# Kernel optimization log

Hardware: AMD Instinct MI355X
Metric: run time of the kernel (lower is better)

## Reference

```python
import jax, jax.numpy as jnp
import numpy as np

GROUP = 128  # quantization group size along the input dimension


def dequant(q, scales, zeros):
    # q: [out, in] int4 codes stored as int32 in [0,16)
    # scales, zeros: [out, in//GROUP] per-group affine params
    out_dim, in_dim = q.shape
    g = in_dim // GROUP
    w = (q.astype(jnp.float32).reshape(out_dim, g, GROUP) - zeros[:, :, None]) * scales[:, :, None]
    return w.reshape(out_dim, in_dim)


def setup_inputs() -> dict:
    key = jax.random.key(0)
    ks = jax.random.split(key, 10)
    H, I = 4096, 11008
    B, S = 64, 1
    inp = {
        "x": jax.random.normal(ks[0], (B, S, H), dtype=jnp.float32),
        "gate_qweight": jax.random.randint(ks[1], (I, H), 0, 16, dtype=jnp.int32),
        "gate_scales": jax.random.uniform(ks[2], (I, H // GROUP), dtype=jnp.float32) * 0.02,
        "gate_zeros": jax.random.uniform(ks[3], (I, H // GROUP), dtype=jnp.float32) * 16.0,
        "up_qweight": jax.random.randint(ks[4], (I, H), 0, 16, dtype=jnp.int32),
        "up_scales": jax.random.uniform(ks[5], (I, H // GROUP), dtype=jnp.float32) * 0.02,
        "up_zeros": jax.random.uniform(ks[6], (I, H // GROUP), dtype=jnp.float32) * 16.0,
        "down_qweight": jax.random.randint(ks[7], (H, I), 0, 16, dtype=jnp.int32),
        "down_scales": jax.random.uniform(ks[8], (H, I // GROUP), dtype=jnp.float32) * 0.02,
        "down_zeros": jax.random.uniform(ks[9], (H, I // GROUP), dtype=jnp.float32) * 16.0,
    }
    return inp


def reference(x, gate_qweight, gate_scales, gate_zeros,
              up_qweight, up_scales, up_zeros,
              down_qweight, down_scales, down_zeros):
    Wg = dequant(gate_qweight, gate_scales, gate_zeros)   # [I, H]
    Wu = dequant(up_qweight, up_scales, up_zeros)         # [I, H]
    Wd = dequant(down_qweight, down_scales, down_zeros)   # [H, I]
    gate = jnp.einsum('bsh,ih->bsi', x, Wg)
    up = jnp.einsum('bsh,ih->bsi', x, Wu)
    h = jax.nn.silu(gate) * up                             # SwiGLU
    return jnp.einsum('bsi,hi->bsh', h, Wd)
```

## Files before the change

kernel.cpp:

```cpp
#include <hip/hip_runtime.h>
#include <hip/hip_bf16.h>
#include <stdint.h>

#define H_DIM 4096
#define I_DIM 11008
#define NGH   32
#define NGI   86
#define KWH   512
#define KWI   1376
#define NWV   5636096

typedef __attribute__((ext_vector_type(8))) short short8;
typedef __attribute__((ext_vector_type(4))) short s16x4;
typedef __attribute__((ext_vector_type(4))) float f32x4;
typedef __attribute__((ext_vector_type(4))) int   i32x4;

static __device__ __forceinline__ short f2bf(float f) {
  union { __hip_bfloat16 b; short s; } u;
  u.b = __float2bfloat16(f);
  return u.s;
}

__global__ void xcvt_kernel(const float* __restrict__ x, short* __restrict__ xb) {
  int i = (blockIdx.x * 256 + threadIdx.x) * 4;
  f32x4 v = *(const f32x4*)(x + i);
  s16x4 o;
  o[0] = f2bf(v[0]); o[1] = f2bf(v[1]); o[2] = f2bf(v[2]); o[3] = f2bf(v[3]);
  *(s16x4*)(xb + i) = o;
}

__global__ __launch_bounds__(256) void packt_kernel(
    const int* __restrict__ gq, const int* __restrict__ uq, const int* __restrict__ dq,
    int* __restrict__ pkt) {
  __shared__ unsigned short sb[16][72];
  int bid = blockIdx.x;
  const int* src; int RL, KW; size_t obase; int rt, ct;
  if (bid < 11008) {
    src = gq; RL = H_DIM; KW = KWH; obase = 0;
    rt = bid >> 4; ct = bid & 15;
  } else if (bid < 22016) {
    src = uq; RL = H_DIM; KW = KWH; obase = (size_t)NWV;
    bid -= 11008; rt = bid >> 4; ct = bid & 15;
  } else {
    src = dq; RL = I_DIM; KW = KWI; obase = 2 * (size_t)NWV;
    bid -= 22016; rt = bid / 43; ct = bid - rt * 43;
  }
  const int t = threadIdx.x;
  const int rowl = t >> 4, j = t & 15;
  const int* rp = src + (size_t)(rt * 16 + rowl) * RL + ct * 256;
#pragma unroll
  for (int p = 0; p < 4; ++p) {
    i32x4 v = *(const i32x4*)(rp + p * 64 + j * 4);
    sb[rowl][p * 16 + j] = (unsigned short)((v[0] & 15) | ((v[1] & 15) << 4)
                        | ((v[2] & 15) << 8) | ((v[3] & 15) << 12));
  }
  __syncthreads();
  int* dst = pkt + obase + ((size_t)rt * KW + ct * 32) * 16;
#pragma unroll
  for (int p = 0; p < 2; ++p) {
    const int wi = t + p * 256;
    const int kwl = wi >> 4, ri = wi & 15;
    dst[wi] = (int)sb[ri][2 * kwl] | ((int)sb[ri][2 * kwl + 1] << 16);
  }
}

__global__ __launch_bounds__(512, 4) void phase1p_kernel(
    const short* __restrict__ xb, const int* __restrict__ pkt,
    const float* __restrict__ gsc, const float* __restrict__ gze,
    const float* __restrict__ usc, const float* __restrict__ uze,
    short* __restrict__ hb)
{
  __shared__ float red[8][4][4][64];
  const int rt   = blockIdx.x;
  const int n0   = rt * 16;
  const int w    = threadIdx.x >> 6;
  const int l    = threadIdx.x & 63;
  const int col  = l & 15;
  const int krow = l >> 4;
  const int i    = n0 + col;

  const int* gB = pkt + (size_t)rt * (KWH * 16) + col;
  const int* uB = pkt + (size_t)NWV + (size_t)rt * (KWH * 16) + col;

  float sgv[4], zgv[4], suv[4], zuv[4];
#pragma unroll
  for (int g = 0; g < 4; ++g) {
    const int gg = w * 4 + g;
    sgv[g] = gsc[(size_t)i * NGH + gg];
    zgv[g] = gze[(size_t)i * NGH + gg] * sgv[g];
    suv[g] = usc[(size_t)i * NGH + gg];
    zuv[g] = uze[(size_t)i * NGH + gg] * suv[g];
  }

  f32x4 accG[4], accU[4];
#pragma unroll
  for (int c = 0; c < 4; ++c)
#pragma unroll
    for (int r = 0; r < 4; ++r) { accG[c][r] = 0.f; accU[c][r] = 0.f; }

  const int wb  = w * 64;
  const int ks0 = w * 512 + krow * 8;

  int qgA = gB[(wb + krow) * 16], quA = uB[(wb + krow) * 16];
  int qgB_, quB_;
  short8 aA[4], aB[4];
#pragma unroll
  for (int c = 0; c < 4; ++c)
    aA[c] = *(const short8*)(xb + (size_t)(c * 16 + col) * H_DIM + ks0);

#pragma unroll
  for (int u = 0; u < 8; ++u) {
    const int t1 = 2 * u + 1;
    const int t2 = (2 * u + 2) & 15;
    const int g  = u >> 1;
    qgB_ = gB[(wb + 4 * t1 + krow) * 16];
    quB_ = uB[(wb + 4 * t1 + krow) * 16];
#pragma unroll
    for (int c = 0; c < 4; ++c)
      aB[c] = *(const short8*)(xb + (size_t)(c * 16 + col) * H_DIM + ks0 + t1 * 32);
    {
      short8 bg, bu;
#pragma unroll
      for (int j = 0; j < 8; ++j) {
        bg[j] = f2bf((float)((qgA >> (4 * j)) & 15) * sgv[g] - zgv[g]);
        bu[j] = f2bf((float)((quA >> (4 * j)) & 15) * suv[g] - zuv[g]);
      }
#pragma unroll
      for (int c = 0; c < 4; ++c) {
        accG[c] = __builtin_amdgcn_mfma_f32_16x16x32_bf16(aA[c], bg, accG[c], 0, 0, 0);
        accU[c] = __builtin_amdgcn_mfma_f32_16x16x32_bf16(aA[c], bu, accU[c], 0, 0, 0);
      }
    }
    qgA = gB[(wb + 4 * t2 + krow) * 16];
    quA = uB[(wb + 4 * t2 + krow) * 16];
#pragma unroll
    for (int c = 0; c < 4; ++c)
      aA[c] = *(const short8*)(xb + (size_t)(c * 16 + col) * H_DIM + ks0 + t2 * 32);
    {
      short8 bg, bu;
#pragma unroll
      for (int j = 0; j < 8; ++j) {
        bg[j] = f2bf((float)((qgB_ >> (4 * j)) & 15) * sgv[g] - zgv[g]);
        bu[j] = f2bf((float)((quB_ >> (4 * j)) & 15) * suv[g] - zuv[g]);
      }
#pragma unroll
      for (int c = 0; c < 4; ++c) {
        accG[c] = __builtin_amdgcn_mfma_f32_16x16x32_bf16(aB[c], bg, accG[c], 0, 0, 0);
        accU[c] = __builtin_amdgcn_mfma_f32_16x16x32_bf16(aB[c], bu, accU[c], 0, 0, 0);
      }
    }
  }

  const int c2 = threadIdx.x >> 7;
  const int rh = (threadIdx.x >> 6) & 1;
  const int ll = threadIdx.x & 63;

#pragma unroll
  for (int c = 0; c < 4; ++c)
#pragma unroll
    for (int r = 0; r < 4; ++r)
      red[w][c][r][l] = accG[c][r];
  __syncthreads();
  float gsum[2];
#pragma unroll
  for (int rr = 0; rr < 2; ++rr) {
    const int r = rh * 2 + rr;
    float s = 0.f;
#pragma unroll
    for (int ww = 0; ww < 8; ++ww) s += red[ww][c2][r][ll];
    gsum[rr] = s;
  }
  __syncthreads();

#pragma unroll
  for (int c = 0; c < 4; ++c)
#pragma unroll
    for (int r = 0; r < 4; ++r)
      red[w][c][r][l] = accU[c][r];
  __syncthreads();
#pragma unroll
  for (int rr = 0; rr < 2; ++rr) {
    const int r = rh * 2 + rr;
    float us = 0.f;
#pragma unroll
    for (int ww = 0; ww < 8; ++ww) us += red[ww][c2][r][ll];
    const float gv = gsum[rr];
    const float hv = gv / (1.f + __expf(-gv)) * us;
    const int m  = c2 * 16 + (ll >> 4) * 4 + r;
    const int ii = n0 + (ll & 15);
    hb[(size_t)m * I_DIM + ii] = f2bf(hv);
  }
}

__global__ __launch_bounds__(512, 4) void phase2p_kernel(
    const short* __restrict__ hb, const int* __restrict__ dpt,
    const float* __restrict__ dsc, const float* __restrict__ dze,
    float* __restrict__ part)
{
  __shared__ float red[8][4][4][64];
  const int tile  = blockIdx.x & 255;
  const int split = blockIdx.x >> 8;
  const int n0   = tile * 16;
  const int w    = threadIdx.x >> 6;
  const int l    = threadIdx.x & 63;
  const int col  = l & 15;
  const int krow = l >> 4;
  const int n    = n0 + col;

  const int* dB = dpt + (size_t)tile * (KWI * 16) + col;

  f32x4 acc[4];
#pragma unroll
  for (int c = 0; c < 4; ++c)
#pragma unroll
    for (int r = 0; r < 4; ++r) acc[c][r] = 0.f;

  const int cnt    = (w < 6) ? 11 : 10;
  const int sstart = (w < 6) ? w * 11 : 66 + (w - 6) * 10;
  const int kbase  = split * 2752 + sstart * 32;
  const int wbase  = split * 344 + sstart * 4;

  const int g0 = kbase >> 7;
  float s0 = dsc[(size_t)n * NGI + g0];
  float s1 = dsc[(size_t)n * NGI + min(g0 + 1, NGI - 1)];
  float s2 = dsc[(size_t)n * NGI + min(g0 + 2, NGI - 1)];
  float s3 = dsc[(size_t)n * NGI + min(g0 + 3, NGI - 1)];
  float z0 = dze[(size_t)n * NGI + g0] * s0;
  float z1 = dze[(size_t)n * NGI + min(g0 + 1, NGI - 1)] * s1;
  float z2 = dze[(size_t)n * NGI + min(g0 + 2, NGI - 1)] * s2;
  float z3 = dze[(size_t)n * NGI + min(g0 + 3, NGI - 1)] * s3;

  int qdA = dB[(wbase + krow) * 16], qdB_;
  short8 aA[4], aB[4];
#pragma unroll
  for (int c = 0; c < 4; ++c)
    aA[c] = *(const short8*)(hb + (size_t)(c * 16 + col) * I_DIM + kbase + krow * 8);

  const int nh = cnt >> 1;
#pragma unroll 1
  for (int u = 0; u < nh; ++u) {
    const int t0 = 2 * u, t1 = 2 * u + 1;
    const int t2 = (t1 + 1 < cnt) ? (t1 + 1) : 0;
    qdB_ = dB[(wbase + 4 * t1 + krow) * 16];
#pragma unroll
    for (int c = 0; c < 4; ++c)
      aB[c] = *(const short8*)(hb + (size_t)(c * 16 + col) * I_DIM + kbase + t1 * 32 + krow * 8);
    {
      const int gi = ((kbase + t0 * 32) >> 7) - g0;
      const float sv = gi == 0 ? s0 : gi == 1 ? s1 : gi == 2 ? s2 : s3;
      const float zv = gi == 0 ? z0 : gi == 1 ? z1 : gi == 2 ? z2 : z3;
      short8 b;
#pragma unroll
      for (int j = 0; j < 8; ++j)
        b[j] = f2bf((float)((qdA >> (4 * j)) & 15) * sv - zv);
#pragma unroll
      for (int c = 0; c < 4; ++c)
        acc[c] = __builtin_amdgcn_mfma_f32_16x16x32_bf16(aA[c], b, acc[c], 0, 0, 0);
    }
    qdA = dB[(wbase + 4 * t2 + krow) * 16];
#pragma unroll
    for (int c = 0; c < 4; ++c)
      aA[c] = *(const short8*)(hb + (size_t)(c * 16 + col) * I_DIM + kbase + t2 * 32 + krow * 8);
    {
      const int gi = ((kbase + t1 * 32) >> 7) - g0;
      const float sv = gi == 0 ? s0 : gi == 1 ? s1 : gi == 2 ? s2 : s3;
      const float zv = gi == 0 ? z0 : gi == 1 ? z1 : gi == 2 ? z2 : z3;
      short8 b;
#pragma unroll
      for (int j = 0; j < 8; ++j)
        b[j] = f2bf((float)((qdB_ >> (4 * j)) & 15) * sv - zv);
#pragma unroll
      for (int c = 0; c < 4; ++c)
        acc[c] = __builtin_amdgcn_mfma_f32_16x16x32_bf16(aB[c], b, acc[c], 0, 0, 0);
    }
  }
  if (cnt & 1) {
    const int t0 = cnt - 1;
    const int gi = ((kbase + t0 * 32) >> 7) - g0;
    const float sv = gi == 0 ? s0 : gi == 1 ? s1 : gi == 2 ? s2 : s3;
    const float zv = gi == 0 ? z0 : gi == 1 ? z1 : gi == 2 ? z2 : z3;
    short8 b;
#pragma unroll
    for (int j = 0; j < 8; ++j)
      b[j] = f2bf((float)((qdA >> (4 * j)) & 15) * sv - zv);
#pragma unroll
    for (int c = 0; c < 4; ++c)
      acc[c] = __builtin_amdgcn_mfma_f32_16x16x32_bf16(aA[c], b, acc[c], 0, 0, 0);
  }

#pragma unroll
  for (int c = 0; c < 4; ++c)
#pragma unroll
    for (int r = 0; r < 4; ++r)
      red[w][c][r][l] = acc[c][r];
  __syncthreads();

  if (threadIdx.x < 256) {
    const int c2 = threadIdx.x >> 6;
    const int ll = threadIdx.x & 63;
    float* po = part + (size_t)split * (64 * H_DIM);
#pragma unroll
    for (int r = 0; r < 4; ++r) {
      float s = 0.f;
#pragma unroll
      for (int ww = 0; ww < 8; ++ww) s += red[ww][c2][r][ll];
      const int m  = c2 * 16 + (ll >> 4) * 4 + r;
      const int nn = n0 + (ll & 15);
      po[(size_t)m * H_DIM + nn] = s;
    }
  }
}

__global__ void reduce4_kernel(const float* __restrict__ part, float* __restrict__ out) {
  const int idx = (blockIdx.x * 256 + threadIdx.x) * 4;
  const int S = 64 * H_DIM;
  f32x4 s0 = *(const f32x4*)(part + idx);
  f32x4 s1 = *(const f32x4*)(part + S + idx);
  f32x4 s2 = *(const f32x4*)(part + 2 * S + idx);
  f32x4 s3 = *(const f32x4*)(part + 3 * S + idx);
  f32x4 r = (s0 + s1) + (s2 + s3);
  *(f32x4*)(out + idx) = r;
}

__global__ __launch_bounds__(512, 4) void phase1f_kernel(
    const short* __restrict__ xb,
    const int* __restrict__ gq, const float* __restrict__ gsc, const float* __restrict__ gze,
    const int* __restrict__ uq, const float* __restrict__ usc, const float* __restrict__ uze,
    short* __restrict__ hb)
{
  __shared__ float red[8][4][4][64];
  const int n0   = blockIdx.x * 16;
  const int w    = threadIdx.x >> 6;
  const int l    = threadIdx.x & 63;
  const int col  = l & 15;
  const int krow = l >> 4;
  const int i    = n0 + col;
  const int*   gqr = gq + (size_t)i * H_DIM;
  const int*   uqr = uq + (size_t)i * H_DIM;
  const float* gsr = gsc + (size_t)i * NGH;
  const float* gzr = gze + (size_t)i * NGH;
  const float* usr = usc + (size_t)i * NGH;
  const float* uzr = uze + (size_t)i * NGH;
  f32x4 accG[4], accU[4];
#pragma unroll
  for (int c = 0; c < 4; ++c)
#pragma unroll
    for (int r = 0; r < 4; ++r) { accG[c][r] = 0.f; accU[c][r] = 0.f; }
  const int kw = w * 512;
#pragma unroll 1
  for (int g = 0; g < 4; ++g) {
    const int gg = w * 4 + g;
    const float sg = gsr[gg], zg = gzr[gg] * sg;
    const float su = usr[gg], zu = uzr[gg] * su;
#pragma unroll
    for (int ks = 0; ks < 4; ++ks) {
      const int koff = kw + g * 128 + ks * 32 + krow * 8;
      i32x4 q0 = *(const i32x4*)(gqr + koff);
      i32x4 q1 = *(const i32x4*)(gqr + koff + 4);
      i32x4 p0 = *(const i32x4*)(uqr + koff);
      i32x4 p1 = *(const i32x4*)(uqr + koff + 4);
      short8 a[4];
#pragma unroll
      for (int c = 0; c < 4; ++c)
        a[c] = *(const short8*)(xb + (size_t)(c * 16 + col) * H_DIM + koff);
      short8 bg, bu;
#pragma unroll
      for (int j = 0; j < 4; ++j) {
        bg[j]     = f2bf((float)q0[j] * sg - zg);
        bg[j + 4] = f2bf((float)q1[j] * sg - zg);
        bu[j]     = f2bf((float)p0[j] * su - zu);
        bu[j + 4] = f2bf((float)p1[j] * su - zu);
      }
#pragma unroll
      for (int c = 0; c < 4; ++c) {
        accG[c] = __builtin_amdgcn_mfma_f32_16x16x32_bf16(a[c], bg, accG[c], 0, 0, 0);
        accU[c] = __builtin_amdgcn_mfma_f32_16x16x32_bf16(a[c], bu, accU[c], 0, 0, 0);
      }
    }
  }
  const int c2 = threadIdx.x >> 7;
  const int rh = (threadIdx.x >> 6) & 1;
  const int ll = threadIdx.x & 63;
#pragma unroll
  for (int c = 0; c < 4; ++c)
#pragma unroll
    for (int r = 0; r < 4; ++r)
      red[w][c][r][l] = accG[c][r];
  __syncthreads();
  float gsum[2];
#pragma unroll
  for (int rr = 0; rr < 2; ++rr) {
    const int r = rh * 2 + rr;
    float s = 0.f;
#pragma unroll
    for (int ww = 0; ww < 8; ++ww) s += red[ww][c2][r][ll];
    gsum[rr] = s;
  }
  __syncthreads();
#pragma unroll
  for (int c = 0; c < 4; ++c)
#pragma unroll
    for (int r = 0; r < 4; ++r)
      red[w][c][r][l] = accU[c][r];
  __syncthreads();
#pragma unroll
  for (int rr = 0; rr < 2; ++rr) {
    const int r = rh * 2 + rr;
    float us = 0.f;
#pragma unroll
    for (int ww = 0; ww < 8; ++ww) us += red[ww][c2][r][ll];
    const float gv = gsum[rr];
    const float hv = gv / (1.f + __expf(-gv)) * us;
    const int m  = c2 * 16 + (ll >> 4) * 4 + r;
    const int ii = n0 + (ll & 15);
    hb[(size_t)m * I_DIM + ii] = f2bf(hv);
  }
}

__global__ __launch_bounds__(512, 4) void phase2f_kernel(
    const short* __restrict__ hb,
    const int* __restrict__ dq, const float* __restrict__ dsc, const float* __restrict__ dze,
    float* __restrict__ part)
{
  __shared__ float red[8][4][4][64];
  const int tile  = blockIdx.x & 255;
  const int split = blockIdx.x >> 8;
  const int n0   = tile * 16;
  const int w    = threadIdx.x >> 6;
  const int l    = threadIdx.x & 63;
  const int col  = l & 15;
  const int krow = l >> 4;
  const int n    = n0 + col;
  const int*   dqr = dq + (size_t)n * I_DIM;
  const float* dsr = dsc + (size_t)n * NGI;
  const float* dzr = dze + (size_t)n * NGI;
  f32x4 acc[4];
#pragma unroll
  for (int c = 0; c < 4; ++c)
#pragma unroll
    for (int r = 0; r < 4; ++r) acc[c][r] = 0.f;
  const int cnt    = (w < 6) ? 11 : 10;
  const int sstart = (w < 6) ? w * 11 : 66 + (w - 6) * 10;
  const int kbase  = split * 2752 + sstart * 32;
  int gprev = -1;
  float sv = 0.f, zv = 0.f;
#pragma unroll 1
  for (int s = 0; s < cnt; ++s) {
    const int k0 = kbase + s * 32;
    const int g  = k0 >> 7;
    if (g != gprev) { sv = dsr[g]; zv = dzr[g] * sv; gprev = g; }
    i32x4 q0 = *(const i32x4*)(dqr + k0 + krow * 8);
    i32x4 q1 = *(const i32x4*)(dqr + k0 + krow * 8 + 4);
    short8 a[4];
#pragma unroll
    for (int c = 0; c < 4; ++c)
      a[c] = *(const short8*)(hb + (size_t)(c * 16 + col) * I_DIM + k0 + krow * 8);
    short8 b;
#pragma unroll
    for (int j = 0; j < 4; ++j) {
      b[j]     = f2bf((float)q0[j] * sv - zv);
      b[j + 4] = f2bf((float)q1[j] * sv - zv);
    }
#pragma unroll
    for (int c = 0; c < 4; ++c)
      acc[c] = __builtin_amdgcn_mfma_f32_16x16x32_bf16(a[c], b, acc[c], 0, 0, 0);
  }
#pragma unroll
  for (int c = 0; c < 4; ++c)
#pragma unroll
    for (int r = 0; r < 4; ++r)
      red[w][c][r][l] = acc[c][r];
  __syncthreads();
  if (threadIdx.x < 256) {
    const int c2 = threadIdx.x >> 6;
    const int ll = threadIdx.x & 63;
    float* po = part + (size_t)split * (64 * H_DIM);
#pragma unroll
    for (int r = 0; r < 4; ++r) {
      float s = 0.f;
#pragma unroll
      for (int ww = 0; ww < 8; ++ww) s += red[ww][c2][r][ll];
      const int m  = c2 * 16 + (ll >> 4) * 4 + r;
      const int nn = n0 + (ll & 15);
      po[(size_t)m * H_DIM + nn] = s;
    }
  }
}

extern "C" void kernel_launch(void* const* d_in, const int* in_sizes, int n_in,
                              void* d_out, int out_size, void* d_ws, size_t ws_size,
                              hipStream_t stream) {
  const float* x  = (const float*)d_in[0];
  const int*   gq = (const int*)d_in[1];
  const float* gs = (const float*)d_in[2];
  const float* gz = (const float*)d_in[3];
  const int*   uq = (const int*)d_in[4];
  const float* us = (const float*)d_in[5];
  const float* uz = (const float*)d_in[6];
  const int*   dq = (const int*)d_in[7];
  const float* ds = (const float*)d_in[8];
  const float* dz = (const float*)d_in[9];
  float* out = (float*)d_out;

  const size_t XB   = (size_t)64 * H_DIM * 2;
  const size_t HB   = (size_t)64 * I_DIM * 2;
  const size_t PART = (size_t)4 * 64 * H_DIM * 4;
  const size_t PK   = (size_t)NWV * 4;

  short* xb   = (short*)d_ws;
  short* hb   = (short*)((char*)d_ws + XB);
  float* part = (float*)((char*)d_ws + XB + HB);
  int*   pkt  = (int*)((char*)d_ws + XB + HB + PART);

  xcvt_kernel<<<(64 * H_DIM) / 1024, 256, 0, stream>>>(x, xb);

  if (ws_size >= XB + HB + PART + 3 * PK) {
    packt_kernel<<<33024, 256, 0, stream>>>(gq, uq, dq, pkt);
    phase1p_kernel<<<I_DIM / 16, 512, 0, stream>>>(xb, pkt, gs, gz, us, uz, hb);
    phase2p_kernel<<<(H_DIM / 16) * 4, 512, 0, stream>>>(hb, pkt + 2 * (size_t)NWV, ds, dz, part);
  } else {
    phase1f_kernel<<<I_DIM / 16, 512, 0, stream>>>(xb, gq, gs, gz, uq, us, uz, hb);
    phase2f_kernel<<<(H_DIM / 16) * 4, 512, 0, stream>>>(hb, dq, ds, dz, part);
  }
  reduce4_kernel<<<(64 * H_DIM) / 1024, 256, 0, stream>>>(part, out);
}
```

Measured before the change: 221.2 us.

## Widen gate/up GEMM tile to 32 columns and fold x conversion into pack kernel

The gate/up fused GEMM now computes two 16-column tiles per block, so each loaded x fragment feeds twice as many MFMAs. The grid shrinks from 688 to 344 blocks, and occupancy hints drop to 2 waves per SIMD. The x-to-bf16 conversion is merged into the weight packing kernel as extra blocks to remove one launch. The trade-off is higher register pressure and fewer blocks to spread across the CUs.

Result: faster. 216.3 us (-2.2%).

```diff
diff --git a/kernel.cpp b/kernel.cpp
--- a/kernel.cpp
+++ b/kernel.cpp
@@ -21,19 +21,20 @@
   return u.s;
 }
 
-__global__ void xcvt_kernel(const float* __restrict__ x, short* __restrict__ xb) {
-  int i = (blockIdx.x * 256 + threadIdx.x) * 4;
-  f32x4 v = *(const f32x4*)(x + i);
-  s16x4 o;
-  o[0] = f2bf(v[0]); o[1] = f2bf(v[1]); o[2] = f2bf(v[2]); o[3] = f2bf(v[3]);
-  *(s16x4*)(xb + i) = o;
-}
-
-__global__ __launch_bounds__(256) void packt_kernel(
+__global__ __launch_bounds__(256) void packall_kernel(
     const int* __restrict__ gq, const int* __restrict__ uq, const int* __restrict__ dq,
-    int* __restrict__ pkt) {
+    int* __restrict__ pkt, const float* __restrict__ x, short* __restrict__ xb)
+{
   __shared__ unsigned short sb[16][72];
   int bid = blockIdx.x;
+  if (bid >= 33024) {
+    const int i = ((bid - 33024) * 256 + threadIdx.x) * 4;
+    f32x4 v = *(const f32x4*)(x + i);
+    s16x4 o;
+    o[0] = f2bf(v[0]); o[1] = f2bf(v[1]); o[2] = f2bf(v[2]); o[3] = f2bf(v[3]);
+    *(s16x4*)(xb + i) = o;
+    return;
+  }
   const int* src; int RL, KW; size_t obase; int rt, ct;
   if (bid < 11008) {
     src = gq; RL = H_DIM; KW = KWH; obase = 0;
@@ -64,45 +65,54 @@
   }
 }
 
-__global__ __launch_bounds__(512, 4) void phase1p_kernel(
-    const short* __restrict__ xb, const int* __restrict__ pkt,
+__global__ __launch_bounds__(512, 2) void gemm_gu_fused(
+    const short* __restrict__ xb,
+    const int* __restrict__ gp, const int* __restrict__ upk,
     const float* __restrict__ gsc, const float* __restrict__ gze,
     const float* __restrict__ usc, const float* __restrict__ uze,
     short* __restrict__ hb)
 {
   __shared__ float red[8][4][4][64];
-  const int rt   = blockIdx.x;
-  const int n0   = rt * 16;
+  const int rtb  = blockIdx.x;
+  const int n0   = rtb * 32;
   const int w    = threadIdx.x >> 6;
   const int l    = threadIdx.x & 63;
   const int col  = l & 15;
   const int krow = l >> 4;
-  const int i    = n0 + col;
-
-  const int* gB = pkt + (size_t)rt * (KWH * 16) + col;
-  const int* uB = pkt + (size_t)NWV + (size_t)rt * (KWH * 16) + col;
-
-  float sgv[4], zgv[4], suv[4], zuv[4];
-#pragma unroll
-  for (int g = 0; g < 4; ++g) {
-    const int gg = w * 4 + g;
-    sgv[g] = gsc[(size_t)i * NGH + gg];
-    zgv[g] = gze[(size_t)i * NGH + gg] * sgv[g];
-    suv[g] = usc[(size_t)i * NGH + gg];
-    zuv[g] = uze[(size_t)i * NGH + gg] * suv[g];
-  }
-
-  f32x4 accG[4], accU[4];
-#pragma unroll
-  for (int c = 0; c < 4; ++c)
-#pragma unroll
-    for (int r = 0; r < 4; ++r) { accG[c][r] = 0.f; accU[c][r] = 0.f; }
+
+  const int* Bg0 = gp  + (size_t)(2 * rtb)     * (KWH * 16) + col;
+  const int* Bg1 = gp  + (size_t)(2 * rtb + 1) * (KWH * 16) + col;
+  const int* Bu0 = upk + (size_t)(2 * rtb)     * (KWH * 16) + col;
+  const int* Bu1 = upk + (size_t)(2 * rtb + 1) * (KWH * 16) + col;
+
+  float sg[2][4], zg[2][4], su[2][4], zu[2][4];
+#pragma unroll
+  for (int cg = 0; cg < 2; ++cg) {
+    const int i = n0 + cg * 16 + col;
+#pragma unroll
+    for (int g = 0; g < 4; ++g) {
+      const int gg = w * 4 + g;
+      sg[cg][g] = gsc[(size_t)i * NGH + gg];
+      zg[cg][g] = gze[(size_t)i * NGH + gg] * sg[cg][g];
+      su[cg][g] = usc[(size_t)i * NGH + gg];
+      zu[cg][g] = uze[(size_t)i * NGH + gg] * su[cg][g];
+    }
+  }
+
+  f32x4 accG[2][4], accU[2][4];
+#pragma unroll
+  for (int cg = 0; cg < 2; ++cg)
+#pragma unroll
+    for (int c = 0; c < 4; ++c)
+#pragma unroll
+      for (int r = 0; r < 4; ++r) { accG[cg][c][r] = 0.f; accU[cg][c][r] = 0.f; }
 
   const int wb  = w * 64;
   const int ks0 = w * 512 + krow * 8;
 
-  int qgA = gB[(wb + krow) * 16], quA = uB[(wb + krow) * 16];
-  int qgB_, quB_;
+  int g0A = Bg0[(wb + krow) * 16], g1A = Bg1[(wb + krow) * 16];
+  int u0A = Bu0[(wb + krow) * 16], u1A = Bu1[(wb + krow) * 16];
+  int g0B, g1B, u0B, u1B;
   short8 aA[4], aB[4];
 #pragma unroll
   for (int c = 0; c < 4; ++c)
@@ -113,40 +123,52 @@
     const int t1 = 2 * u + 1;
     const int t2 = (2 * u + 2) & 15;
     const int g  = u >> 1;
-    qgB_ = gB[(wb + 4 * t1 + krow) * 16];
-    quB_ = uB[(wb + 4 * t1 + krow) * 16];
+    g0B = Bg0[(wb + 4 * t1 + krow) * 16];
+    g1B = Bg1[(wb + 4 * t1 + krow) * 16];
+    u0B = Bu0[(wb + 4 * t1 + krow) * 16];
+    u1B = Bu1[(wb + 4 * t1 + krow) * 16];
 #pragma unroll
     for (int c = 0; c < 4; ++c)
       aB[c] = *(const short8*)(xb + (size_t)(c * 16 + col) * H_DIM + ks0 + t1 * 32);
     {
-      short8 bg, bu;
+      short8 bg0, bg1, bu0, bu1;
 #pragma unroll
       for (int j = 0; j < 8; ++j) {
-        bg[j] = f2bf((float)((qgA >> (4 * j)) & 15) * sgv[g] - zgv[g]);
-        bu[j] = f2bf((float)((quA >> (4 * j)) & 15) * suv[g] - zuv[g]);
+        bg0[j] = f2bf((float)((g0A >> (4 * j)) & 15) * sg[0][g] - zg[0][g]);
+        bg1[j] = f2bf((float)((g1A >> (4 * j)) & 15) * sg[1][g] - zg[1][g]);
+        bu0[j] = f2bf((float)((u0A >> (4 * j)) & 15) * su[0][g] - zu[0][g]);
+        bu1[j] = f2bf((float)((u1A >> (4 * j)) & 15) * su[1][g] - zu[1][g]);
       }
 #pragma unroll
       for (int c = 0; c < 4; ++c) {
-        accG[c] = __builtin_amdgcn_mfma_f32_16x16x32_bf16(aA[c], bg, accG[c], 0, 0, 0);
-        accU[c] = __builtin_amdgcn_mfma_f32_16x16x32_bf16(aA[c], bu, accU[c], 0, 0, 0);
+        accG[0][c] = __builtin_amdgcn_mfma_f32_16x16x32_bf16(aA[c], bg0, accG[0][c], 0, 0, 0);
+        accG[1][c] = __builtin_amdgcn_mfma_f32_16x16x32_bf16(aA[c], bg1, accG[1][c], 0, 0, 0);
+        accU[0][c] = __builtin_amdgcn_mfma_f32_16x16x32_bf16(aA[c], bu0, accU[0][c], 0, 0, 0);
+        accU[1][c] = __builtin_amdgcn_mfma_f32_16x16x32_bf16(aA[c], bu1, accU[1][c], 0, 0, 0);
       }
     }
-    qgA = gB[(wb + 4 * t2 + krow) * 16];
-    quA = uB[(wb + 4 * t2 + krow) * 16];
+    g0A = Bg0[(wb + 4 * t2 + krow) * 16];
+    g1A = Bg1[(wb + 4 * t2 + krow) * 16];
+    u0A = Bu0[(wb + 4 * t2 + krow) * 16];
+    u1A = Bu1[(wb + 4 * t2 + krow) * 16];
 #pragma unroll
     for (int c = 0; c < 4; ++c)
       aA[c] = *(const short8*)(xb + (size_t)(c * 16 + col) * H_DIM + ks0 + t2 * 32);
     {
-      short8 bg, bu;
+      short8 bg0, bg1, bu0, bu1;
 #pragma unroll
       for (int j = 0; j < 8; ++j) {
-        bg[j] = f2bf((float)((qgB_ >> (4 * j)) & 15) * sgv[g] - zgv[g]);
-        bu[j] = f2bf((float)((quB_ >> (4 * j)) & 15) * suv[g] - zuv[g]);
+        bg0[j] = f2bf((float)((g0B >> (4 * j)) & 15) * sg[0][g] - zg[0][g]);
+        bg1[j] = f2bf((float)((g1B >> (4 * j)) & 15) * sg[1][g] - zg[1][g]);
+        bu0[j] = f2bf((float)((u0B >> (4 * j)) & 15) * su[0][g] - zu[0][g]);
+        bu1[j] = f2bf((float)((u1B >> (4 * j)) & 15) * su[1][g] - zu[1][g]);
       }
 #pragma unroll
       for (int c = 0; c < 4; ++c) {
-        accG[c] = __builtin_amdgcn_mfma_f32_16x16x32_bf16(aB[c], bg, accG[c], 0, 0, 0);
-        accU[c] = __builtin_amdgcn_mfma_f32_16x16x32_bf16(aB[c], bu, accU[c], 0, 0, 0);
+        accG[0][c] = __builtin_amdgcn_mfma_f32_16x16x32_bf16(aB[c], bg0, accG[0][c], 0, 0, 0);
+        accG[1][c] = __builtin_amdgcn_mfma_f32_16x16x32_bf16(aB[c], bg1, accG[1][c], 0, 0, 0);
+        accU[0][c] = __builtin_amdgcn_mfma_f32_16x16x32_bf16(aB[c], bu0, accU[0][c], 0, 0, 0);
+        accU[1][c] = __builtin_amdgcn_mfma_f32_16x16x32_bf16(aB[c], bu1, accU[1][c], 0, 0, 0);
       }
     }
   }
@@ -154,41 +176,43 @@
   const int c2 = threadIdx.x >> 7;
   const int rh = (threadIdx.x >> 6) & 1;
   const int ll = threadIdx.x & 63;
-
-#pragma unroll
-  for (int c = 0; c < 4; ++c)
-#pragma unroll
-    for (int r = 0; r < 4; ++r)
-      red[w][c][r][l] = accG[c][r];
-  __syncthreads();
-  float gsum[2];
-#pragma unroll
-  for (int rr = 0; rr < 2; ++rr) {
-    const int r = rh * 2 + rr;
-    float s = 0.f;
-#pragma unroll
-    for (int ww = 0; ww < 8; ++ww) s += red[ww][c2][r][ll];
-    gsum[rr] = s;
-  }
-  __syncthreads();
-
-#pragma unroll
-  for (int c = 0; c < 4; ++c)
-#pragma unroll
-    for (int r = 0; r < 4; ++r)
-      red[w][c][r][l] = accU[c][r];
-  __syncthreads();
-#pragma unroll
-  for (int rr = 0; rr < 2; ++rr) {
-    const int r = rh * 2 + rr;
-    float us = 0.f;
-#pragma unroll
-    for (int ww = 0; ww < 8; ++ww) us += red[ww][c2][r][ll];
-    const float gv = gsum[rr];
-    const float hv = gv / (1.f + __expf(-gv)) * us;
-    const int m  = c2 * 16 + (ll >> 4) * 4 + r;
-    const int ii = n0 + (ll & 15);
-    hb[(size_t)m * I_DIM + ii] = f2bf(hv);
+#pragma unroll
+  for (int cg = 0; cg < 2; ++cg) {
+#pragma unroll
+    for (int c = 0; c < 4; ++c)
+#pragma unroll
+      for (int r = 0; r < 4; ++r)
+        red[w][c][r][l] = accG[cg][c][r];
+    __syncthreads();
+    float gsumr[2];
+#pragma unroll
+    for (int rr = 0; rr < 2; ++rr) {
+      const int r = rh * 2 + rr;
+      float s = 0.f;
+#pragma unroll
+      for (int ww = 0; ww < 8; ++ww) s += red[ww][c2][r][ll];
+      gsumr[rr] = s;
+    }
+    __syncthreads();
+#pragma unroll
+    for (int c = 0; c < 4; ++c)
+#pragma unroll
+      for (int r = 0; r < 4; ++r)
+        red[w][c][r][l] = accU[cg][c][r];
+    __syncthreads();
+#pragma unroll
+    for (int rr = 0; rr < 2; ++rr) {
+      const int r = rh * 2 + rr;
+      float us = 0.f;
+#pragma unroll
+      for (int ww = 0; ww < 8; ++ww) us += red[ww][c2][r][ll];
+      const float gv = gsumr[rr];
+      const float hv = gv / (1.f + __expf(-gv)) * us;
+      const int m  = c2 * 16 + (ll >> 4) * 4 + r;
+      const int ii = n0 + cg * 16 + (ll & 15);
+      hb[(size_t)m * I_DIM + ii] = f2bf(hv);
+    }
+    if (cg == 0) __syncthreads();
   }
 }
 
@@ -320,6 +344,14 @@
   f32x4 s3 = *(const f32x4*)(part + 3 * S + idx);
   f32x4 r = (s0 + s1) + (s2 + s3);
   *(f32x4*)(out + idx) = r;
+}
+
+__global__ void xcvt_kernel(const float* __restrict__ x, short* __restrict__ xb) {
+  int i = (blockIdx.x * 256 + threadIdx.x) * 4;
+  f32x4 v = *(const f32x4*)(x + i);
+  s16x4 o;
+  o[0] = f2bf(v[0]); o[1] = f2bf(v[1]); o[2] = f2bf(v[2]); o[3] = f2bf(v[3]);
+  *(s16x4*)(xb + i) = o;
 }
 
 __global__ __launch_bounds__(512, 4) void phase1f_kernel(
@@ -511,14 +543,16 @@
   short* hb   = (short*)((char*)d_ws + XB);
   float* part = (float*)((char*)d_ws + XB + HB);
   int*   pkt  = (int*)((char*)d_ws + XB + HB + PART);
-
-  xcvt_kernel<<<(64 * H_DIM) / 1024, 256, 0, stream>>>(x, xb);
+  int*   gp   = pkt;
+  int*   upk  = pkt + (size_t)NWV;
+  int*   dpk  = pkt + 2 * (size_t)NWV;
 
   if (ws_size >= XB + HB + PART + 3 * PK) {
-    packt_kernel<<<33024, 256, 0, stream>>>(gq, uq, dq, pkt);
-    phase1p_kernel<<<I_DIM / 16, 512, 0, stream>>>(xb, pkt, gs, gz, us, uz, hb);
-    phase2p_kernel<<<(H_DIM / 16) * 4, 512, 0, stream>>>(hb, pkt + 2 * (size_t)NWV, ds, dz, part);
+    packall_kernel<<<33024 + 256, 256, 0, stream>>>(gq, uq, dq, pkt, x, xb);
+    gemm_gu_fused<<<344, 512, 0, stream>>>(xb, gp, upk, gs, gz, us, uz, hb);
+    phase2p_kernel<<<(H_DIM / 16) * 4, 512, 0, stream>>>(hb, dpk, ds, dz, part);
   } else {
+    xcvt_kernel<<<(64 * H_DIM) / 1024, 256, 0, stream>>>(x, xb);
     phase1f_kernel<<<I_DIM / 16, 512, 0, stream>>>(xb, gq, gs, gz, uq, us, uz, hb);
     phase2f_kernel<<<(H_DIM / 16) * 4, 512, 0, stream>>>(hb, dq, ds, dz, part);
   }
```
